# Kernel tuning notes

Hardware: AMD Instinct MI355X
Metric: run time of the kernel (lower is better)

The kernel has to match this reference:

```python
import jax, jax.numpy as jnp
import numpy as np

# LIF constants matching SpikingLinearLayer defaults
DT = 1.0
TAU_M = 20.0
TAU_S = 5.0
THRESH = 1.0
SURR_BETA = 10.0  # surrogate sigmoid sharpness


def _spike(v):
    """Hard threshold forward, sigmoid surrogate gradient (straight-through)."""
    s_hard = (v >= 0.0).astype(v.dtype)
    s_surr = jax.nn.sigmoid(SURR_BETA * v)
    return s_surr + jax.lax.stop_gradient(s_hard - s_surr)


def setup_inputs() -> dict:
    key = jax.random.key(0)
    k1, k2 = jax.random.split(key)
    T, B, IN, OUT = 20, 1024, 2048, 2048
    x = (jax.random.uniform(k1, (T, B, IN)) < 0.1).astype(jnp.float32)
    # nn.init.normal_(weight, mu=0.1, std=0.1)
    weight = 0.1 + 0.1 * jax.random.normal(k2, (OUT, IN), dtype=jnp.float32)
    return {"x": x, "weight": weight}


def reference(x, weight):
    # x: [T, B, in_dim] spike trains; weight: [out_dim, in_dim]
    alpha_m = 1.0 - DT / TAU_M  # membrane decay
    alpha_s = 1.0 - DT / TAU_S  # synaptic decay
    # batch all timestep GEMMs into one contraction: [T, B, out]
    cur = jnp.einsum("tbi,oi->tbo", x, weight)
    B, O = cur.shape[1], cur.shape[2]
    V0 = jnp.zeros((B, O), cur.dtype)
    I0 = jnp.zeros((B, O), cur.dtype)

    def step(carry, c_t):
        V, I = carry
        I = alpha_s * I + c_t                   # tau_s dI/dt = -I + W s_in
        V = alpha_m * V + (DT / TAU_M) * I      # tau_m dV/dt = -V + I
        s = _spike(V - THRESH)                  # fire at threshold
        V = V * (1.0 - s)                       # reset to zero on spike
        return (V, I), s

    _, spikes = jax.lax.scan(step, (V0, I0), cur)
    return spikes  # [T, B, out_dim]
```

## Files before the change

### kernel.cpp

```cpp
#include <hip/hip_runtime.h>
#include <stdint.h>


constexpr int T_STEPS = 20;
constexpr int BATCH   = 1024;
constexpr int NIN     = 2048;
constexpr int NOUT    = 2048;

constexpr int    Q         = 4;
constexpr double SCALE     = 1073741824.0;
constexpr double INV_SCALE = 1.0 / SCALE;

constexpr size_t XIP_BYTES   = (size_t)T_STEPS * 16 * 1024 * 16;
constexpr size_t PLANE_BYTES = (size_t)NOUT * NIN;
constexpr size_t WS_NEEDED   = XIP_BYTES + (size_t)Q * PLANE_BYTES;

typedef int v4i __attribute__((ext_vector_type(4)));

__device__ __forceinline__ void dma16(const int8_t* g, const int8_t* l) {
    __builtin_amdgcn_global_load_lds(
        (const __attribute__((address_space(1))) void*)(uintptr_t)g,
        (__attribute__((address_space(3))) void*)(uint32_t)(uintptr_t)l,
        16, 0, 0);
}

__device__ __forceinline__ v4i expand16(uint32_t b) {
    v4i r;
    r[0] = (int)(__umul24((b      ) & 0xFu, 0x00204081u) & 0x01010101u);
    r[1] = (int)(__umul24((b >>  4) & 0xFu, 0x00204081u) & 0x01010101u);
    r[2] = (int)(__umul24((b >>  8) & 0xFu, 0x00204081u) & 0x01010101u);
    r[3] = (int)(__umul24((b >> 12) & 0xFu, 0x00204081u) & 0x01010101u);
    return r;
}

__global__ void prep_x(const float* __restrict__ x, int8_t* __restrict__ xp) {
    const int tid  = threadIdx.x;
    const int ln   = tid & 63;
    const int row  = blockIdx.x * 4 + (tid >> 6);
    const int t    = row >> 10;
    const int b    = row & 1023;
    const float* xr = x + (size_t)row * NIN;
#pragma unroll
    for (int c = 0; c < 32; ++c) {
        const unsigned long long m = __ballot(xr[c * 64 + ln] != 0.0f);
        if (ln == 0)
            *reinterpret_cast<unsigned long long*>(
                xp + (((size_t)t * 16 + (c >> 1)) * 1024 + b) * 16
                   + (c & 1) * 8) = m;
    }
}

__global__ void prep_limbs(const float* __restrict__ w, int8_t* __restrict__ limbs) {
    const int idx = blockIdx.x * blockDim.x + threadIdx.x;
    const float4 wv = reinterpret_cast<const float4*>(w)[idx];
    const float wf[4] = {wv.x, wv.y, wv.z, wv.w};
    int8_t d[Q][4];
#pragma unroll
    for (int e = 0; e < 4; ++e) {
        long long M = llrint((double)wf[e] * SCALE);
#pragma unroll
        for (int j = 0; j < Q - 1; ++j) {
            const int dj = (int)((M + 128) & 255) - 128;
            d[j][e] = (int8_t)dj;
            M = (M - dj) >> 8;
        }
        d[Q - 1][e] = (int8_t)M;
    }
#pragma unroll
    for (int j = 0; j < Q; ++j)
        reinterpret_cast<char4*>(limbs + (size_t)j * PLANE_BYTES)[idx] =
            make_char4(d[j][0], d[j][1], d[j][2], d[j][3]);
}

constexpr int KC2    = 256;
constexpr int NKC2   = NIN / KC2;
constexpr int TT     = 4;
constexpr int NTQ    = T_STEPS / TT;
constexpr int NITER  = NTQ * NKC2;
constexpr int BM     = 256;
constexpr int BO     = 16;
constexpr int B_OFF  = 32768;
constexpr int BUF_B  = 49152;

constexpr ptrdiff_t DA_STEP = 32768;
constexpr ptrdiff_t DA_WRAP = 819200;
constexpr ptrdiff_t DB_STEP = 256;
constexpr ptrdiff_t DB_WRAP = -1792;

__global__ __launch_bounds__(512, 2)
void snn_i8(const int8_t* __restrict__ xp, const int8_t* __restrict__ limbs,
            float* __restrict__ out)
{
    const int bid   = blockIdx.x;
    const int xcd   = bid & 7;
    const int sub   = bid >> 3;
    const int otile = xcd * 16 + (sub & 15);
    const int btile = sub >> 4;
    const int o0 = otile * BO, b0 = btile * BM;

    const int tid = threadIdx.x;
    const int w   = tid >> 6;
    const int ln  = tid & 63;
    const int lm  = ln & 15;
    const int qd  = ln >> 4;

    __shared__ __align__(16) int8_t lds[2][BUF_B];

    const int sa_tt = w >> 1;
    const int sa_h  = w & 1;
    const int sb_j  = w >> 1;
    const int sb_kq = w & 1;

    const int8_t* a_nxt = xp
        + ((size_t)(sa_tt * 16 + sa_h)) * 16384 + (size_t)(b0 + ln) * 16;
    const int8_t* b_nxt = limbs + (size_t)sb_j * PLANE_BYTES
        + (size_t)(o0 + lm) * NIN + sb_kq * 128 + qd * 16;

    double V[8], I[8];
#pragma unroll
    for (int e = 0; e < 8; ++e) { V[e] = 0.0; I[e] = 0.0; }

    const double alpha_m = 1.0 - 1.0 / 20.0;
    const double alpha_s = 1.0 - 1.0 / 5.0;
    const double dtm     = 1.0 / 20.0;

    auto stageN = [&](int par) {
        int8_t* lb = &lds[par][0];
#pragma unroll
        for (int g = 0; g < 4; ++g)
            dma16(a_nxt + g * 1024,
                  lb + sa_tt * 8192 + sa_h * 4096 + g * 1024);
#pragma unroll
        for (int c = 0; c < 2; ++c)
            dma16(b_nxt + c * 64,
                  lb + B_OFF + (sb_j * 4 + sb_kq * 2 + c) * 1024);
    };

    stageN(0);
    a_nxt += DA_STEP;
    b_nxt += DB_STEP;
    __syncthreads();

    int s = 0;
    for (int tq = 0; tq < NTQ; ++tq) {
        v4i acc[2][4][4];
#pragma unroll
        for (int rg2 = 0; rg2 < 2; ++rg2)
#pragma unroll
            for (int tt = 0; tt < TT; ++tt)
#pragma unroll
                for (int j = 0; j < Q; ++j)
                    acc[rg2][tt][j] = (v4i){0, 0, 0, 0};

        for (int kci = 0; kci < NKC2; ++kci, ++s) {
            if (s + 1 < NITER) stageN((s + 1) & 1);
            {
                const bool wr = (kci == NKC2 - 2);
                a_nxt += wr ? DA_WRAP : DA_STEP;
                b_nxt += wr ? DB_WRAP : DB_STEP;
            }

            const int8_t* cb = &lds[s & 1][0];
#pragma unroll
            for (int s2 = 0; s2 < 4; ++s2) {
                v4i B[4];
#pragma unroll
                for (int j = 0; j < Q; ++j)
                    B[j] = *reinterpret_cast<const v4i*>(
                        cb + B_OFF + (j * 4 + s2) * 1024 + ln * 16);
#pragma unroll
                for (int rg2 = 0; rg2 < 2; ++rg2) {
                    const int r = (2 * w + rg2) * 16 + lm;
#pragma unroll
                    for (int tt = 0; tt < TT; ++tt) {
                        const uint32_t bits =
                            *reinterpret_cast<const uint16_t*>(
                                cb + tt * 8192 + (s2 >> 1) * 4096 + r * 16
                                   + (s2 & 1) * 8 + qd * 2);
                        const v4i A = expand16(bits);
#pragma unroll
                        for (int j = 0; j < Q; ++j)
                            acc[rg2][tt][j] =
                                __builtin_amdgcn_mfma_i32_16x16x64_i8(
                                    A, B[j], acc[rg2][tt][j], 0, 0, 0);
                    }
                }
            }
            __syncthreads();
        }

        const int ocol = o0 + lm;
#pragma unroll
        for (int rg2 = 0; rg2 < 2; ++rg2) {
#pragma unroll
            for (int r = 0; r < 4; ++r) {
                const int e = rg2 * 4 + r;
                const int brow = b0 + (2 * w + rg2) * 16 + 4 * qd + r;
#pragma unroll
                for (int tt = 0; tt < TT; ++tt) {
                    const int d0 = acc[rg2][tt][0][r];
                    const int d1 = acc[rg2][tt][1][r];
                    const int d2 = acc[rg2][tt][2][r];
                    const int d3 = acc[rg2][tt][3][r];
                    double sm = (double)d3;
                    sm = sm * 256.0 + (double)d2;
                    sm = sm * 256.0 + (double)d1;
                    sm = sm * 256.0 + (double)d0;
                    const double cur = sm * INV_SCALE;

                    I[e] = alpha_s * I[e] + cur;
                    V[e] = alpha_m * V[e] + dtm * I[e];
                    const double sp = (V[e] >= 1.0) ? 1.0 : 0.0;
                    V[e] *= (1.0 - sp);

                    __builtin_nontemporal_store(
                        (float)sp,
                        out + (size_t)(tq * 4 + tt) * BATCH * NOUT
                            + (size_t)brow * NOUT + ocol);
                }
            }
        }
    }
}

constexpr int TBF = 64, TOF = 64, KCF = 64, LDPF = KCF + 4;

__global__ __launch_bounds__(256, 2)
void snn_fused(const float* __restrict__ x,
               const float* __restrict__ w,
               float* __restrict__ out)
{
    const int o0  = blockIdx.x * TOF;
    const int b0  = blockIdx.y * TBF;
    const int tid = threadIdx.x;
    const int tx  = tid & 15;
    const int ty  = tid >> 4;

    __shared__ float xs[TBF][LDPF];
    __shared__ float ws[TOF][LDPF];

    const int lr = tid >> 2;
    const int lc = (tid & 3) << 4;

    double V[4][4], I[4][4];
#pragma unroll
    for (int i = 0; i < 4; ++i)
#pragma unroll
        for (int j = 0; j < 4; ++j) { V[i][j] = 0.0; I[i][j] = 0.0; }

    const double alpha_m = 1.0 - 1.0 / 20.0;
    const double alpha_s = 1.0 - 1.0 / 5.0;
    const double dtm     = 1.0 / 20.0;

    for (int t = 0; t < T_STEPS; ++t) {
        const float* xt = x + (size_t)t * BATCH * NIN;
        double c[4][4];
#pragma unroll
        for (int i = 0; i < 4; ++i)
#pragma unroll
            for (int j = 0; j < 4; ++j) c[i][j] = 0.0;

        for (int kc = 0; kc < NIN; kc += KCF) {
            __syncthreads();
            {
                const float4* xg = reinterpret_cast<const float4*>(
                    xt + (size_t)(b0 + lr) * NIN + kc + lc);
                const float4* wg = reinterpret_cast<const float4*>(
                    w + (size_t)(o0 + lr) * NIN + kc + lc);
#pragma unroll
                for (int q = 0; q < 4; ++q) {
                    float4 xv = xg[q];
                    float4 wv4 = wg[q];
                    const int cbi = lc + q * 4;
                    xs[lr][cbi + 0] = xv.x;  xs[lr][cbi + 1] = xv.y;
                    xs[lr][cbi + 2] = xv.z;  xs[lr][cbi + 3] = xv.w;
                    ws[lr][cbi + 0] = wv4.x; ws[lr][cbi + 1] = wv4.y;
                    ws[lr][cbi + 2] = wv4.z; ws[lr][cbi + 3] = wv4.w;
                }
            }
            __syncthreads();

#pragma unroll 8
            for (int k = 0; k < KCF; ++k) {
                float xa[4], wa[4];
#pragma unroll
                for (int i = 0; i < 4; ++i) xa[i] = xs[ty * 4 + i][k];
#pragma unroll
                for (int j = 0; j < 4; ++j) wa[j] = ws[tx * 4 + j][k];
#pragma unroll
                for (int i = 0; i < 4; ++i)
#pragma unroll
                    for (int j = 0; j < 4; ++j)
                        c[i][j] += (double)xa[i] * (double)wa[j];
            }
        }

#pragma unroll
        for (int i = 0; i < 4; ++i) {
            float sv[4];
#pragma unroll
            for (int j = 0; j < 4; ++j) {
                I[i][j] = alpha_s * I[i][j] + c[i][j];
                V[i][j] = alpha_m * V[i][j] + dtm * I[i][j];
                const double sp = (V[i][j] >= 1.0) ? 1.0 : 0.0;
                V[i][j] *= (1.0 - sp);
                sv[j] = (float)sp;
            }
            const size_t oidx = (size_t)t * BATCH * NOUT
                              + (size_t)(b0 + ty * 4 + i) * NOUT
                              + (size_t)(o0 + tx * 4);
            *reinterpret_cast<float4*>(out + oidx) =
                make_float4(sv[0], sv[1], sv[2], sv[3]);
        }
    }
}

extern "C" void kernel_launch(void* const* d_in, const int* in_sizes, int n_in,
                              void* d_out, int out_size, void* d_ws, size_t ws_size,
                              hipStream_t stream) {
    const float* x = (const float*)d_in[0];
    const float* w = (const float*)d_in[1];
    float* out     = (float*)d_out;
    (void)in_sizes; (void)n_in; (void)out_size;

    if (ws_size >= WS_NEEDED) {
        int8_t* xp    = (int8_t*)d_ws;
        int8_t* limbs = xp + XIP_BYTES;
        prep_x<<<5120, 256, 0, stream>>>(x, xp);
        prep_limbs<<<(int)(PLANE_BYTES / 4 / 256), 256, 0, stream>>>(w, limbs);
        snn_i8<<<512, 512, 0, stream>>>(xp, limbs, out);
    } else {
        dim3 grid(NOUT / TOF, BATCH / TBF);
        snn_fused<<<grid, dim3(256), 0, stream>>>(x, w, out);
    }
}
```

Before: 556.7 us.

## Hoist B fragments, load A as 16-byte vectors, spill V state to LDS

The inner K loop now loads all 16 B fragments up front and reads each A tile row as two 16-byte LDS loads, extracting the per-lane 16-bit spike masks with shifts. Previously it issued many 2-byte LDS reads. MFMA groups are wrapped in s_setprio to favour matrix issue. The membrane potential V is kept in a 32 KB LDS array instead of registers, freeing VGPRs for the larger B fragment set. The extra LDS footprint may cut the number of resident blocks, and the LDS round trips add epilogue latency.

```diff
diff --git a/kernel.cpp b/kernel.cpp
--- a/kernel.cpp
+++ b/kernel.cpp
@@ -103,8 +103,14 @@
     const int ln  = tid & 63;
     const int lm  = ln & 15;
     const int qd  = ln >> 4;
+    const int qdh = qd >> 1;
+    const int qdo = qd & 1;
 
     __shared__ __align__(16) int8_t lds[2][BUF_B];
+    __shared__ double ldsV[8][512];
+
+#pragma unroll
+    for (int e = 0; e < 8; ++e) ldsV[e][tid] = 0.0;
 
     const int sa_tt = w >> 1;
     const int sa_h  = w & 1;
@@ -116,9 +122,9 @@
     const int8_t* b_nxt = limbs + (size_t)sb_j * PLANE_BYTES
         + (size_t)(o0 + lm) * NIN + sb_kq * 128 + qd * 16;
 
-    double V[8], I[8];
-#pragma unroll
-    for (int e = 0; e < 8; ++e) { V[e] = 0.0; I[e] = 0.0; }
+    double I[8];
+#pragma unroll
+    for (int e = 0; e < 8; ++e) I[e] = 0.0;
 
     const double alpha_m = 1.0 - 1.0 / 20.0;
     const double alpha_s = 1.0 - 1.0 / 5.0;
@@ -161,28 +167,46 @@
             }
 
             const int8_t* cb = &lds[s & 1][0];
-#pragma unroll
-            for (int s2 = 0; s2 < 4; ++s2) {
-                v4i B[4];
-#pragma unroll
-                for (int j = 0; j < Q; ++j)
-                    B[j] = *reinterpret_cast<const v4i*>(
+
+            v4i Bf[4][4];
+#pragma unroll
+            for (int j = 0; j < Q; ++j)
+#pragma unroll
+                for (int s2 = 0; s2 < 4; ++s2)
+                    Bf[j][s2] = *reinterpret_cast<const v4i*>(
                         cb + B_OFF + (j * 4 + s2) * 1024 + ln * 16);
-#pragma unroll
-                for (int rg2 = 0; rg2 < 2; ++rg2) {
-                    const int r = (2 * w + rg2) * 16 + lm;
-#pragma unroll
-                    for (int tt = 0; tt < TT; ++tt) {
-                        const uint32_t bits =
-                            *reinterpret_cast<const uint16_t*>(
-                                cb + tt * 8192 + (s2 >> 1) * 4096 + r * 16
-                                   + (s2 & 1) * 8 + qd * 2);
-                        const v4i A = expand16(bits);
-#pragma unroll
-                        for (int j = 0; j < Q; ++j)
-                            acc[rg2][tt][j] =
-                                __builtin_amdgcn_mfma_i32_16x16x64_i8(
-                                    A, B[j], acc[rg2][tt][j], 0, 0, 0);
+
+#pragma unroll
+            for (int rg2 = 0; rg2 < 2; ++rg2) {
+                const int r = (2 * w + rg2) * 16 + lm;
+#pragma unroll
+                for (int tt = 0; tt < TT; ++tt) {
+                    const v4i a0 = *reinterpret_cast<const v4i*>(
+                        cb + tt * 8192 + 0    + r * 16);
+                    const v4i a1 = *reinterpret_cast<const v4i*>(
+                        cb + tt * 8192 + 4096 + r * 16);
+#pragma unroll
+                    for (int g = 0; g < 2; ++g) {
+                        const v4i ag = g ? a1 : a0;
+                        const uint32_t dwE =
+                            (uint32_t)(qdh ? ag[1] : ag[0]);
+                        const uint32_t dwO =
+                            (uint32_t)(qdh ? ag[3] : ag[2]);
+#pragma unroll
+                        for (int p = 0; p < 2; ++p) {
+                            const int s2 = 2 * g + p;
+                            const uint32_t dw = p ? dwO : dwE;
+                            const uint32_t e16 = qdo ? (dw >> 16) : dw;
+                            const v4i A = expand16(e16);
+                            __builtin_amdgcn_s_setprio(1);
+#pragma unroll
+                            for (int j = 0; j < Q; ++j)
+                                acc[rg2][tt][j] =
+                                    __builtin_amdgcn_mfma_i32_16x16x64_i8(
+                                        A, Bf[j][s2], acc[rg2][tt][j],
+                                        0, 0, 0);
+                            __builtin_amdgcn_s_setprio(0);
+                        }
                     }
                 }
             }
@@ -196,6 +220,7 @@
             for (int r = 0; r < 4; ++r) {
                 const int e = rg2 * 4 + r;
                 const int brow = b0 + (2 * w + rg2) * 16 + 4 * qd + r;
+                double Vv = ldsV[e][tid];
 #pragma unroll
                 for (int tt = 0; tt < TT; ++tt) {
                     const int d0 = acc[rg2][tt][0][r];
@@ -209,15 +234,16 @@
                     const double cur = sm * INV_SCALE;
 
                     I[e] = alpha_s * I[e] + cur;
-                    V[e] = alpha_m * V[e] + dtm * I[e];
-                    const double sp = (V[e] >= 1.0) ? 1.0 : 0.0;
-                    V[e] *= (1.0 - sp);
+                    Vv   = alpha_m * Vv + dtm * I[e];
+                    const double sp = (Vv >= 1.0) ? 1.0 : 0.0;
+                    Vv *= (1.0 - sp);
 
                     __builtin_nontemporal_store(
                         (float)sp,
                         out + (size_t)(tq * 4 + tt) * BATCH * NOUT
                             + (size_t)brow * NOUT + ocol);
                 }
+                ldsV[e][tid] = Vv;
             }
         }
     }
```

Result: slower. 574.2 us (+3.1%).
